# Performance work log

Hardware: AMD Instinct MI355X
Metric: run time of the kernel (lower is better)

## Reference

```python
import jax, jax.numpy as jnp
import numpy as np
import math

N = 50000
E = 600000
HID = 128
NG = 50
NF = 128
CUTOFF = 10.0
OFFSET = 0.0


def ssp(x):
    # shifted softplus, standard SchNet activation
    return jax.nn.softplus(x) - jnp.log(2.0).astype(x.dtype)


def setup_inputs() -> dict:
    key = jax.random.key(0)
    ks = jax.random.split(key, 12)
    x = jax.random.normal(ks[0], (N, HID), dtype=jnp.float32)
    ji_pairs = jax.random.randint(ks[1], (2, E), 0, N, dtype=jnp.int64)
    e_ji = jax.random.uniform(ks[2], (E,), dtype=jnp.float32) * CUTOFF
    e_ji_basis = jax.random.normal(ks[3], (E, NG), dtype=jnp.float32)
    # filter_nn: Linear(NG, NF) -> ssp -> Linear(NF, NF)
    fw1 = jax.random.normal(ks[4], (NF, NG), dtype=jnp.float32) * (1.0 / np.sqrt(NG))
    fb1 = jnp.zeros((NF,), jnp.float32)
    fw2 = jax.random.normal(ks[5], (NF, NF), dtype=jnp.float32) * (1.0 / np.sqrt(NF))
    fb2 = jnp.zeros((NF,), jnp.float32)
    # CFConv linear1 (no bias), linear2
    w1 = jax.random.normal(ks[6], (NF, HID), dtype=jnp.float32) * (1.0 / np.sqrt(HID))
    w2 = jax.random.normal(ks[7], (HID, NF), dtype=jnp.float32) * (1.0 / np.sqrt(NF))
    b2 = jnp.zeros((HID,), jnp.float32)
    # InteractionBlock linear3
    w3 = jax.random.normal(ks[8], (HID, HID), dtype=jnp.float32) * (1.0 / np.sqrt(HID))
    b3 = jnp.zeros((HID,), jnp.float32)
    return {"x": x, "ji_pairs": ji_pairs, "e_ji": e_ji, "e_ji_basis": e_ji_basis,
            "fw1": fw1, "fb1": fb1, "fw2": fw2, "fb2": fb2,
            "w1": w1, "w2": w2, "b2": b2, "w3": w3, "b3": b3}


def reference(x, ji_pairs, e_ji, e_ji_basis, fw1, fb1, fw2, fb2, w1, w2, b2, w3, b3):
    # cosine cutoff  [E]
    C = 0.25 * (jnp.cos((e_ji - OFFSET) * (np.pi / (CUTOFF - OFFSET))) + 1.0)
    # filter MLP on edge basis  [E, NF]
    h = ssp(e_ji_basis @ fw1.T + fb1)
    W = (h @ fw2.T + fb2) * C[:, None]
    # node projection  [N, NF]
    xh = x @ w1.T
    # gather x_j, modulate by W, scatter-add to target nodes (PyG source_to_target)
    src, dst = ji_pairs[0], ji_pairs[1]
    msg = xh[src] * W                                # [E, NF]
    agg = jax.ops.segment_sum(msg, dst, num_segments=N)  # [N, NF]
    out = agg @ w2.T + b2                            # [N, HID]
    out = ssp(out)
    out = out @ w3.T + b3
    return out
```

## Files before the change

kernel.cpp:

```cpp
#include <hip/hip_runtime.h>

typedef float f32x4 __attribute__((ext_vector_type(4)));
typedef short bf16x8 __attribute__((ext_vector_type(8)));
typedef unsigned short u16;
typedef unsigned int u32;

__device__ __forceinline__ u32 cvt_pk_bf16(float lo, float hi) {
    u32 r;
    asm("v_cvt_pk_bf16_f32 %0, %1, %2" : "=v"(r) : "v"(lo), "v"(hi));
    return r;
}

__device__ __forceinline__ u16 f2b(float f) {
    union { float f; u32 u; } v; v.f = f;
    u32 r = v.u + 0x7fffu + ((v.u >> 16) & 1u);
    return (u16)(r >> 16);
}
__device__ __forceinline__ float b2f_lo(u32 p) {
    union { u32 u; float f; } v; v.u = p << 16; return v.f;
}
__device__ __forceinline__ float b2f_hi(u32 p) {
    union { u32 u; float f; } v; v.u = p & 0xffff0000u; return v.f;
}

__device__ __forceinline__ float ssp(float x) {
    return fmaxf(x, 0.0f) + __logf(1.0f + __expf(-fabsf(x))) - 0.6931471805599453f;
}

__global__ void prep_weights(const float* __restrict__ fw1,
                             const float* __restrict__ fw2,
                             const float* __restrict__ w1,
                             const float* __restrict__ w2,
                             const float* __restrict__ w3,
                             u16* __restrict__ out) {
    int t = blockIdx.x * blockDim.x + threadIdx.x;
    if (t < 128 * 64) {
        int c = t >> 6, k = t & 63;
        out[t] = f2b(k < 50 ? fw1[c * 50 + k] : 0.0f);
        return;
    }
    t -= 128 * 64;
    if (t < 16384) { out[8192 + t] = f2b(fw2[t]); return; }
    t -= 16384;
    if (t < 16384) { out[8192 + 16384 + t] = f2b(w1[t]); return; }
    t -= 16384;
    if (t < 16384) { out[8192 + 32768 + t] = f2b(w2[t]); return; }
    t -= 16384;
    if (t < 16384) { out[8192 + 49152 + t] = f2b(w3[t]); return; }
}

template <int ACT, int OBF>
__global__ __launch_bounds__(256, 3) void linear128(
    const float* __restrict__ in, const u16* __restrict__ wb,
    const float* __restrict__ bias, void* __restrict__ outv, int M) {
    __shared__ u16 in_lds[64 * 136];
    __shared__ u16 w_lds[128 * 136];

    const int tid = threadIdx.x;
    const int r0 = blockIdx.x * 64;

    for (int idx = tid; idx < 128 * 16; idx += 256) {
        int c = idx >> 4, kc = (idx & 15) * 8;
        *reinterpret_cast<uint4*>(&w_lds[c * 136 + kc]) =
            *reinterpret_cast<const uint4*>(&wb[c * 128 + kc]);
    }
    for (int idx = tid; idx < 64 * 32; idx += 256) {
        int r = idx >> 5, kc = (idx & 31) * 4;
        int row = r0 + r;
        float4 v = make_float4(0.f, 0.f, 0.f, 0.f);
        if (row < M) v = *reinterpret_cast<const float4*>(&in[(size_t)row * 128 + kc]);
        u32* p = reinterpret_cast<u32*>(&in_lds[r * 136 + kc]);
        p[0] = cvt_pk_bf16(v.x, v.y); p[1] = cvt_pk_bf16(v.z, v.w);
    }
    __syncthreads();

    const int l = tid & 63, w = tid >> 6;
    const int lr = l & 15, lg = l >> 4;

    f32x4 acc[8] = {};
    for (int ks = 0; ks < 4; ++ks) {
        bf16x8 a = *reinterpret_cast<const bf16x8*>(
            &in_lds[(w * 16 + lr) * 136 + ks * 32 + lg * 8]);
        for (int n = 0; n < 8; ++n) {
            bf16x8 b = *reinterpret_cast<const bf16x8*>(
                &w_lds[(n * 16 + lr) * 136 + ks * 32 + lg * 8]);
            acc[n] = __builtin_amdgcn_mfma_f32_16x16x32_bf16(a, b, acc[n], 0, 0, 0);
        }
    }

    for (int n = 0; n < 8; ++n) {
        int c = n * 16 + lr;
        float bv = bias ? bias[c] : 0.0f;
        for (int i = 0; i < 4; ++i) {
            int row = r0 + w * 16 + lg * 4 + i;
            if (row < M) {
                float v = acc[n][i] + bv;
                if (ACT) v = ssp(v);
                if (OBF) ((u16*)outv)[(size_t)row * 128 + c] = f2b(v);
                else     ((float*)outv)[(size_t)row * 128 + c] = v;
            }
        }
    }
}

__global__ __launch_bounds__(512) void edge_mlp(
    const float* __restrict__ basis, const float* __restrict__ e_ji,
    const u16* __restrict__ fw1b, const u16* __restrict__ fw2b,
    const float* __restrict__ fb1, const float* __restrict__ fb2,
    const int* __restrict__ epos, u16* __restrict__ Wb,
    int E, int nTiles, int stride) {
    __shared__ u16 bas[2][32 * 72];
    __shared__ u16 hb[2][32 * 136];

    const int tid = threadIdx.x;
    const int l = tid & 63, w = tid >> 6;
    const int lr = l & 15, lg = l >> 4;
    const int c8 = lg * 8, c4 = lg * 4;

    bf16x8 wa1[2], wa2[4];
    const u16* p1 = &fw1b[(size_t)(w * 16 + lr) * 64];
    wa1[0] = *reinterpret_cast<const bf16x8*>(p1 + c8);
    wa1[1] = *reinterpret_cast<const bf16x8*>(p1 + 32 + c8);
    const u16* p2 = &fw2b[(size_t)(w * 16 + lr) * 128];
#pragma unroll
    for (int ks = 0; ks < 4; ++ks)
        wa2[ks] = *reinterpret_cast<const bf16x8*>(p2 + ks * 32 + c8);
    const float4 b1v = *reinterpret_cast<const float4*>(&fb1[w * 16 + c4]);
    const float4 b2v = *reinterpret_cast<const float4*>(&fb2[w * 16 + c4]);

    for (int idx = tid; idx < 2 * 32 * 7; idx += 512) {
        int b = idx / 224, rem = idx - b * 224;
        int row = rem / 7, q = rem - row * 7;
        *reinterpret_cast<u32*>(&bas[b][row * 72 + 50 + 2 * q]) = 0u;
    }

    const int srow = tid & 31, cb = tid >> 5;
    const bool has2 = cb < 9;

    int it = blockIdx.x;
    if (it >= nTiles) return;

    {
        int er = it * 32 + srow; if (er >= E) er = E - 1;
        const float* rp = &basis[(size_t)er * 50];
        float2 v0 = *reinterpret_cast<const float2*>(rp + 2 * cb);
        *reinterpret_cast<u32*>(&bas[0][srow * 72 + 2 * cb]) = cvt_pk_bf16(v0.x, v0.y);
        if (has2) {
            float2 v1 = *reinterpret_cast<const float2*>(rp + 2 * (cb + 16));
            *reinterpret_cast<u32*>(&bas[0][srow * 72 + 2 * (cb + 16)]) =
                cvt_pk_bf16(v1.x, v1.y);
        }
    }
    __syncthreads();

    int buf = 0;
    for (; it < nTiles; it += stride, buf ^= 1) {
        const int nxt = it + stride;
        const bool hn = nxt < nTiles;
        float2 stg0, stg1;
        if (hn) {
            int er = nxt * 32 + srow; if (er >= E) er = E - 1;
            const float* rp = &basis[(size_t)er * 50];
            stg0 = *reinterpret_cast<const float2*>(rp + 2 * cb);
            if (has2) stg1 = *reinterpret_cast<const float2*>(rp + 2 * (cb + 16));
        }
        const int er0 = it * 32 + lr, er1 = er0 + 16;
        const int ec0 = er0 < E ? er0 : E - 1;
        const int ec1 = er1 < E ? er1 : E - 1;
        const int ep0 = epos[ec0], ep1 = epos[ec1];
        const float ej0 = e_ji[ec0], ej1 = e_ji[ec1];

        f32x4 acc1[2] = {};
#pragma unroll
        for (int ks = 0; ks < 2; ++ks) {
            bf16x8 bb0 = *reinterpret_cast<const bf16x8*>(
                &bas[buf][lr * 72 + ks * 32 + c8]);
            bf16x8 bb1 = *reinterpret_cast<const bf16x8*>(
                &bas[buf][(16 + lr) * 72 + ks * 32 + c8]);
            acc1[0] = __builtin_amdgcn_mfma_f32_16x16x32_bf16(wa1[ks], bb0, acc1[0], 0, 0, 0);
            acc1[1] = __builtin_amdgcn_mfma_f32_16x16x32_bf16(wa1[ks], bb1, acc1[1], 0, 0, 0);
        }
#pragma unroll
        for (int t = 0; t < 2; ++t) {
            u32* d = reinterpret_cast<u32*>(
                &hb[buf][(t * 16 + lr) * 136 + w * 16 + c4]);
            d[0] = cvt_pk_bf16(ssp(acc1[t][0] + b1v.x), ssp(acc1[t][1] + b1v.y));
            d[1] = cvt_pk_bf16(ssp(acc1[t][2] + b1v.z), ssp(acc1[t][3] + b1v.w));
        }
        if (hn) {
            *reinterpret_cast<u32*>(&bas[buf ^ 1][srow * 72 + 2 * cb]) =
                cvt_pk_bf16(stg0.x, stg0.y);
            if (has2)
                *reinterpret_cast<u32*>(&bas[buf ^ 1][srow * 72 + 2 * (cb + 16)]) =
                    cvt_pk_bf16(stg1.x, stg1.y);
        }
        __syncthreads();

        f32x4 acc2[2] = {};
#pragma unroll
        for (int ks = 0; ks < 4; ++ks) {
            bf16x8 hb0 = *reinterpret_cast<const bf16x8*>(
                &hb[buf][lr * 136 + ks * 32 + c8]);
            bf16x8 hb1 = *reinterpret_cast<const bf16x8*>(
                &hb[buf][(16 + lr) * 136 + ks * 32 + c8]);
            acc2[0] = __builtin_amdgcn_mfma_f32_16x16x32_bf16(wa2[ks], hb0, acc2[0], 0, 0, 0);
            acc2[1] = __builtin_amdgcn_mfma_f32_16x16x32_bf16(wa2[ks], hb1, acc2[1], 0, 0, 0);
        }
#pragma unroll
        for (int t = 0; t < 2; ++t) {
            const int er = t == 0 ? er0 : er1;
            if (er < E) {
                const float ej = t == 0 ? ej0 : ej1;
                const int pos = t == 0 ? ep0 : ep1;
                const float cv = 0.25f * (__cosf(ej * 0.31415926535897932f) + 1.0f);
                uint2 pk;
                pk.x = cvt_pk_bf16((acc2[t][0] + b2v.x) * cv,
                                   (acc2[t][1] + b2v.y) * cv);
                pk.y = cvt_pk_bf16((acc2[t][2] + b2v.z) * cv,
                                   (acc2[t][3] + b2v.w) * cv);
                *reinterpret_cast<uint2*>(
                    &Wb[(size_t)pos * 128 + w * 16 + c4]) = pk;
            }
        }
    }
}

__global__ __launch_bounds__(256) void fused_tail(
    const float* __restrict__ agg, const u16* __restrict__ w2b,
    const u16* __restrict__ w3b, const float* __restrict__ b2,
    const float* __restrict__ b3, float* __restrict__ out,
    int N, int nTiles, int stride) {
    __shared__ u16 bas[2][32 * 136];
    __shared__ u16 hb[2][32 * 136];

    const int tid = threadIdx.x;
    const int l = tid & 63, w = tid >> 6;
    const int lr = l & 15, lg = l >> 4;
    const int c8 = lg * 8, c4 = lg * 4;

    bf16x8 wA[2][4], wB[2][4];
    float4 b2v[2], b3v[2];
#pragma unroll
    for (int i = 0; i < 2; ++i) {
        const u16* pA = &w2b[(size_t)((w * 2 + i) * 16 + lr) * 128];
        const u16* pB = &w3b[(size_t)((w * 2 + i) * 16 + lr) * 128];
#pragma unroll
        for (int ks = 0; ks < 4; ++ks) {
            wA[i][ks] = *reinterpret_cast<const bf16x8*>(pA + ks * 32 + c8);
            wB[i][ks] = *reinterpret_cast<const bf16x8*>(pB + ks * 32 + c8);
        }
        b2v[i] = *reinterpret_cast<const float4*>(&b2[(w * 2 + i) * 16 + c4]);
        b3v[i] = *reinterpret_cast<const float4*>(&b3[(w * 2 + i) * 16 + c4]);
    }

    const int srow = tid & 31, cb = tid >> 5;

    int it = blockIdx.x;
    if (it >= nTiles) return;

    {
        int nd = it * 32 + srow; if (nd >= N) nd = N - 1;
        const float* rp = &agg[(size_t)nd * 128];
#pragma unroll
        for (int r = 0; r < 8; ++r) {
            int c = cb + r * 8;
            float2 v = *reinterpret_cast<const float2*>(rp + 2 * c);
            *reinterpret_cast<u32*>(&bas[0][srow * 136 + 2 * c]) =
                cvt_pk_bf16(v.x, v.y);
        }
    }
    __syncthreads();

    int buf = 0;
    for (; it < nTiles; it += stride, buf ^= 1) {
        const int nxt = it + stride;
        const bool hn = nxt < nTiles;
        float2 stg[8];
        if (hn) {
            int nd = nxt * 32 + srow; if (nd >= N) nd = N - 1;
            const float* rp = &agg[(size_t)nd * 128];
#pragma unroll
            for (int r = 0; r < 8; ++r)
                stg[r] = *reinterpret_cast<const float2*>(rp + 2 * (cb + r * 8));
        }

        f32x4 acc1[2][2] = {};
#pragma unroll
        for (int ks = 0; ks < 4; ++ks) {
            bf16x8 bb0 = *reinterpret_cast<const bf16x8*>(
                &bas[buf][lr * 136 + ks * 32 + c8]);
            bf16x8 bb1 = *reinterpret_cast<const bf16x8*>(
                &bas[buf][(16 + lr) * 136 + ks * 32 + c8]);
#pragma unroll
            for (int i = 0; i < 2; ++i) {
                acc1[0][i] = __builtin_amdgcn_mfma_f32_16x16x32_bf16(wA[i][ks], bb0, acc1[0][i], 0, 0, 0);
                acc1[1][i] = __builtin_amdgcn_mfma_f32_16x16x32_bf16(wA[i][ks], bb1, acc1[1][i], 0, 0, 0);
            }
        }
#pragma unroll
        for (int t = 0; t < 2; ++t) {
#pragma unroll
            for (int i = 0; i < 2; ++i) {
                u32* d = reinterpret_cast<u32*>(
                    &hb[buf][(t * 16 + lr) * 136 + (w * 2 + i) * 16 + c4]);
                d[0] = cvt_pk_bf16(ssp(acc1[t][i][0] + b2v[i].x),
                                   ssp(acc1[t][i][1] + b2v[i].y));
                d[1] = cvt_pk_bf16(ssp(acc1[t][i][2] + b2v[i].z),
                                   ssp(acc1[t][i][3] + b2v[i].w));
            }
        }
        if (hn) {
#pragma unroll
            for (int r = 0; r < 8; ++r)
                *reinterpret_cast<u32*>(&bas[buf ^ 1][srow * 136 + 2 * (cb + r * 8)]) =
                    cvt_pk_bf16(stg[r].x, stg[r].y);
        }
        __syncthreads();

        f32x4 acc2[2][2] = {};
#pragma unroll
        for (int ks = 0; ks < 4; ++ks) {
            bf16x8 hb0 = *reinterpret_cast<const bf16x8*>(
                &hb[buf][lr * 136 + ks * 32 + c8]);
            bf16x8 hb1 = *reinterpret_cast<const bf16x8*>(
                &hb[buf][(16 + lr) * 136 + ks * 32 + c8]);
#pragma unroll
            for (int i = 0; i < 2; ++i) {
                acc2[0][i] = __builtin_amdgcn_mfma_f32_16x16x32_bf16(wB[i][ks], hb0, acc2[0][i], 0, 0, 0);
                acc2[1][i] = __builtin_amdgcn_mfma_f32_16x16x32_bf16(wB[i][ks], hb1, acc2[1][i], 0, 0, 0);
            }
        }
#pragma unroll
        for (int t = 0; t < 2; ++t) {
            int nd = it * 32 + t * 16 + lr;
            if (nd < N) {
#pragma unroll
                for (int i = 0; i < 2; ++i) {
                    float4 o;
                    o.x = acc2[t][i][0] + b3v[i].x;
                    o.y = acc2[t][i][1] + b3v[i].y;
                    o.z = acc2[t][i][2] + b3v[i].z;
                    o.w = acc2[t][i][3] + b3v[i].w;
                    *reinterpret_cast<float4*>(
                        &out[(size_t)nd * 128 + (w * 2 + i) * 16 + c4]) = o;
                }
            }
        }
    }
}

__global__ void hist_kernel(const int* __restrict__ pairs, int* __restrict__ deg, int E) {
    int e = blockIdx.x * blockDim.x + threadIdx.x;
    if (e < E) atomicAdd(&deg[pairs[E + e]], 1);
}

__global__ void scan_a(const int* __restrict__ deg, int* __restrict__ incl,
                       int* __restrict__ bsum, int N) {
    __shared__ int s[256];
    int i = blockIdx.x * 256 + threadIdx.x;
    int v = (i < N) ? deg[i] : 0;
    s[threadIdx.x] = v; __syncthreads();
    for (int off = 1; off < 256; off <<= 1) {
        int t = (threadIdx.x >= off) ? s[threadIdx.x - off] : 0;
        __syncthreads();
        s[threadIdx.x] += t; __syncthreads();
    }
    if (i < N) incl[i] = s[threadIdx.x];
    if (threadIdx.x == 255) bsum[blockIdx.x] = s[255];
}

__global__ void scan_b(int* __restrict__ bsum, int nb) {
    __shared__ int s[256];
    int v = (threadIdx.x < nb) ? bsum[threadIdx.x] : 0;
    s[threadIdx.x] = v; __syncthreads();
    for (int off = 1; off < 256; off <<= 1) {
        int t = (threadIdx.x >= off) ? s[threadIdx.x - off] : 0;
        __syncthreads();
        s[threadIdx.x] += t; __syncthreads();
    }
    if (threadIdx.x < nb) bsum[threadIdx.x] = s[threadIdx.x] - v;
}

__global__ void scan_c(const int* __restrict__ incl, const int* __restrict__ deg,
                       const int* __restrict__ bsum, int* __restrict__ rowst,
                       int* __restrict__ cursor, int N) {
    int i = blockIdx.x * 256 + threadIdx.x;
    if (i < N) {
        int r = incl[i] - deg[i] + bsum[blockIdx.x];
        rowst[i] = r; cursor[i] = r;
    }
}

__global__ void fill_kernel(const int* __restrict__ pairs, int* __restrict__ cursor,
                            int* __restrict__ esrc, int* __restrict__ epos, int E) {
    int e = blockIdx.x * blockDim.x + threadIdx.x;
    if (e < E) {
        int s = pairs[e], d = pairs[E + e];
        int pos = atomicAdd(&cursor[d], 1);
        esrc[pos] = s;
        epos[e] = pos;
    }
}

__global__ __launch_bounds__(256) void aggregate(
    const u16* __restrict__ Wb, const u16* __restrict__ xhb,
    const int* __restrict__ rowst, const int* __restrict__ deg,
    const int* __restrict__ esrc, float* __restrict__ agg, int N) {
    const int w = threadIdx.x >> 6, lane = threadIdx.x & 63;
    const int n = blockIdx.x * 4 + w;
    if (n >= N) return;
    const int rs = rowst[n], d = deg[n];
    const int g = lane >> 4;
    const int co = (lane & 15) * 8;
    float acc[8] = {0.f, 0.f, 0.f, 0.f, 0.f, 0.f, 0.f, 0.f};
    const int nq = (d + 3) >> 2;
    const int dm1 = d > 0 ? d - 1 : 0;

    int srcn = (d > 0) ? esrc[rs + (g < d ? g : dm1)] : 0;
    for (int q = 0; q < nq; ++q) {
        const int k = q * 4 + g;
        const bool val = k < d;
        const int row = rs + (val ? k : dm1);
        const int src = srcn;
        const int kn = (q + 1) * 4 + g;
        if (q + 1 < nq) srcn = esrc[rs + (kn < d ? kn : dm1)];

        uint4 wp = *reinterpret_cast<const uint4*>(&Wb[(size_t)row * 128 + co]);
        uint4 xp = *reinterpret_cast<const uint4*>(&xhb[(size_t)src * 128 + co]);
        if (val) {
            const u32* wu = reinterpret_cast<const u32*>(&wp);
            const u32* xu = reinterpret_cast<const u32*>(&xp);
#pragma unroll
            for (int c = 0; c < 4; ++c) {
                acc[2 * c]     = fmaf(b2f_lo(xu[c]), b2f_lo(wu[c]), acc[2 * c]);
                acc[2 * c + 1] = fmaf(b2f_hi(xu[c]), b2f_hi(wu[c]), acc[2 * c + 1]);
            }
        }
    }
#pragma unroll
    for (int c = 0; c < 8; ++c) {
        float v = acc[c];
        v += __shfl_xor(v, 16);
        v += __shfl_xor(v, 32);
        acc[c] = v;
    }
    if (g == 0) {
        float4 o0 = make_float4(acc[0], acc[1], acc[2], acc[3]);
        float4 o1 = make_float4(acc[4], acc[5], acc[6], acc[7]);
        *reinterpret_cast<float4*>(&agg[(size_t)n * 128 + co]) = o0;
        *reinterpret_cast<float4*>(&agg[(size_t)n * 128 + co + 4]) = o1;
    }
}

__global__ __launch_bounds__(256, 2) void edge_kernel(
    const float* __restrict__ basis, const float* __restrict__ e_ji,
    const int* __restrict__ pairs, const float* __restrict__ xh,
    const u16* __restrict__ fw1b, const u16* __restrict__ fw2b,
    const float* __restrict__ fb1, const float* __restrict__ fb2,
    float* __restrict__ agg, int E) {
    __shared__ u16 hb[64 * 136];
    __shared__ u16 fw1_lds[128 * 72];
    __shared__ u16 fw2_lds[128 * 136];
    __shared__ float cc[64];
    __shared__ int s_src[64];
    __shared__ int s_dst[64];

    const int tid = threadIdx.x;
    const int e0 = blockIdx.x * 64;

    for (int idx = tid; idx < 128 * 8; idx += 256) {
        int c = idx >> 3, kc = (idx & 7) * 8;
        *reinterpret_cast<uint4*>(&fw1_lds[c * 72 + kc]) =
            *reinterpret_cast<const uint4*>(&fw1b[c * 64 + kc]);
    }
    for (int idx = tid; idx < 128 * 16; idx += 256) {
        int c = idx >> 4, kc = (idx & 15) * 8;
        *reinterpret_cast<uint4*>(&fw2_lds[c * 136 + kc]) =
            *reinterpret_cast<const uint4*>(&fw2b[c * 128 + kc]);
    }
    for (int idx = tid; idx < 64 * 64; idx += 256) {
        int e = idx >> 6, k = idx & 63;
        int eg = e0 + e;
        float v = (k < 50 && eg < E) ? basis[(size_t)eg * 50 + k] : 0.0f;
        hb[e * 72 + k] = f2b(v);
    }
    if (tid < 64) {
        int eg = e0 + tid;
        if (eg < E) {
            cc[tid] = 0.25f * (__cosf(e_ji[eg] * 0.31415926535897932f) + 1.0f);
            s_src[tid] = pairs[eg];
            s_dst[tid] = pairs[E + eg];
        } else { cc[tid] = 0.0f; s_src[tid] = 0; s_dst[tid] = 0; }
    }
    __syncthreads();

    const int l = tid & 63, w = tid >> 6;
    const int lr = l & 15, lg = l >> 4;

    f32x4 acc1[8] = {};
    for (int ks = 0; ks < 2; ++ks) {
        bf16x8 a = *reinterpret_cast<const bf16x8*>(
            &hb[(w * 16 + lr) * 72 + ks * 32 + lg * 8]);
        for (int n = 0; n < 8; ++n) {
            bf16x8 b = *reinterpret_cast<const bf16x8*>(
                &fw1_lds[(n * 16 + lr) * 72 + ks * 32 + lg * 8]);
            acc1[n] = __builtin_amdgcn_mfma_f32_16x16x32_bf16(a, b, acc1[n], 0, 0, 0);
        }
    }
    __syncthreads();

    for (int n = 0; n < 8; ++n) {
        int c = n * 16 + lr;
        float bv = fb1[c];
        for (int i = 0; i < 4; ++i) {
            int r = w * 16 + lg * 4 + i;
            hb[r * 136 + c] = f2b(ssp(acc1[n][i] + bv));
        }
    }
    __syncthreads();

    f32x4 acc2[8] = {};
    for (int ks = 0; ks < 4; ++ks) {
        bf16x8 a = *reinterpret_cast<const bf16x8*>(
            &hb[(w * 16 + lr) * 136 + ks * 32 + lg * 8]);
        for (int n = 0; n < 8; ++n) {
            bf16x8 b = *reinterpret_cast<const bf16x8*>(
                &fw2_lds[(n * 16 + lr) * 136 + ks * 32 + lg * 8]);
            acc2[n] = __builtin_amdgcn_mfma_f32_16x16x32_bf16(a, b, acc2[n], 0, 0, 0);
        }
    }

    for (int n = 0; n < 8; ++n) {
        int c = n * 16 + lr;
        float bv = fb2[c];
        for (int i = 0; i < 4; ++i) {
            int eloc = w * 16 + lg * 4 + i;
            if (e0 + eloc < E) {
                float Wv = (acc2[n][i] + bv) * cc[eloc];
                float val = xh[(size_t)s_src[eloc] * 128 + c] * Wv;
                unsafeAtomicAdd(&agg[(size_t)s_dst[eloc] * 128 + c], val);
            }
        }
    }
}

extern "C" void kernel_launch(void* const* d_in, const int* in_sizes, int n_in,
                              void* d_out, int out_size, void* d_ws, size_t ws_size,
                              hipStream_t stream) {
    const float* x      = (const float*)d_in[0];
    const int*   pairs  = (const int*)d_in[1];
    const float* e_ji   = (const float*)d_in[2];
    const float* basis  = (const float*)d_in[3];
    const float* fw1    = (const float*)d_in[4];
    const float* fb1    = (const float*)d_in[5];
    const float* fw2    = (const float*)d_in[6];
    const float* fb2    = (const float*)d_in[7];
    const float* w1     = (const float*)d_in[8];
    const float* w2     = (const float*)d_in[9];
    const float* b2     = (const float*)d_in[10];
    const float* w3     = (const float*)d_in[11];
    const float* b3     = (const float*)d_in[12];
    float* out = (float*)d_out;

    const int N = in_sizes[0] / 128;
    const int E = in_sizes[2];
    const int nodeBlocks = (N + 63) / 64;
    const int nchunks = (N + 255) / 256;
    char* ws = (char*)d_ws;

    size_t off = 0;
    auto nxt = [&](size_t bytes) {
        size_t o = off; off = (off + bytes + 255) & ~(size_t)255; return o;
    };
    u16*   Wb     = (u16*)  (ws + nxt((size_t)E * 128 * 2));
    u16*   xhb    = (u16*)  (ws + nxt((size_t)N * 128 * 2));
    float* agg    = (float*)(ws + nxt((size_t)N * 128 * 4));
    u16*   wb     = (u16*)  (ws + nxt(81920 * 2));
    int*   deg    = (int*)  (ws + nxt((size_t)N * 4));
    int*   incl   = (int*)  (ws + nxt((size_t)N * 4));
    int*   rowst  = (int*)  (ws + nxt((size_t)N * 4));
    int*   cursor = (int*)  (ws + nxt((size_t)N * 4));
    int*   bsum   = (int*)  (ws + nxt(1024));
    int*   esrc   = (int*)  (ws + nxt((size_t)E * 4));
    int*   epos   = (int*)  (ws + nxt((size_t)E * 4));
    const size_t needed = off;

    const u16* fw1b = wb;
    const u16* fw2b = wb + 8192;
    const u16* w1b  = wb + 8192 + 16384;
    const u16* w2b  = wb + 8192 + 32768;
    const u16* w3b  = wb + 8192 + 49152;

    if (ws_size >= needed && nchunks <= 256) {
        prep_weights<<<288, 256, 0, stream>>>(fw1, fw2, w1, w2, w3, wb);
        hipMemsetAsync(deg, 0, (size_t)N * 4, stream);

        linear128<0, 1><<<nodeBlocks, 256, 0, stream>>>(x, w1b, nullptr, xhb, N);

        hist_kernel<<<(E + 255) / 256, 256, 0, stream>>>(pairs, deg, E);
        scan_a<<<nchunks, 256, 0, stream>>>(deg, incl, bsum, N);
        scan_b<<<1, 256, 0, stream>>>(bsum, nchunks);
        scan_c<<<nchunks, 256, 0, stream>>>(incl, deg, bsum, rowst, cursor, N);
        fill_kernel<<<(E + 255) / 256, 256, 0, stream>>>(pairs, cursor, esrc, epos, E);

        const int nTiles = (E + 31) / 32;
        const int gridE = nTiles < 1024 ? nTiles : 1024;
        edge_mlp<<<gridE, 512, 0, stream>>>(basis, e_ji, fw1b, fw2b,
                                            fb1, fb2, epos, Wb, E, nTiles, gridE);
        aggregate<<<(N + 3) / 4, 256, 0, stream>>>(Wb, xhb, rowst, deg,
                                                   esrc, agg, N);

        const int ntT = (N + 31) / 32;
        const int gridT = ntT < 1024 ? ntT : 1024;
        fused_tail<<<gridT, 256, 0, stream>>>(agg, w2b, w3b, b2, b3, out,
                                              N, ntT, gridT);
    } else {
        const size_t nodeBytes = (size_t)N * 128 * sizeof(float);
        float* xhf   = (float*)ws;
        float* aggf  = (float*)(ws + nodeBytes);
        u16*   wbf   = (u16*)(ws + 2 * nodeBytes);
        const u16* ffw1b = wbf;
        const u16* ffw2b = wbf + 8192;
        const u16* fw1bw = wbf + 8192 + 16384;
        const u16* fw2bw = wbf + 8192 + 32768;
        const u16* fw3bw = wbf + 8192 + 49152;

        prep_weights<<<288, 256, 0, stream>>>(fw1, fw2, w1, w2, w3, wbf);
        hipMemsetAsync(aggf, 0, nodeBytes, stream);
        linear128<0, 0><<<nodeBlocks, 256, 0, stream>>>(x, fw1bw, nullptr, xhf, N);
        edge_kernel<<<(E + 63) / 64, 256, 0, stream>>>(basis, e_ji, pairs, xhf,
                                                       ffw1b, ffw2b, fb1, fb2, aggf, E);
        linear128<1, 0><<<nodeBlocks, 256, 0, stream>>>(aggf, fw2bw, b2, out, N);
        linear128<0, 0><<<nodeBlocks, 256, 0, stream>>>(out, fw3bw, b3, out, N);
    }
}
```

Before: 276.5 us.

## Fuse CSR aggregation with the two-layer node tail into one kernel

Merges the per-node gather/aggregate kernel with the fused_tail MLP kernel. Each 512-thread block aggregates 32 nodes (4 per wave) into a bf16 LDS tile and then runs the w2/ssp/w3 MFMA chain on it directly. This removes the fp32 agg round trip through global memory and one launch. In exchange it drops the persistent double-buffered tail loop and makes each block finish all of its gather work before any MFMA runs.

```diff
diff --git a/kernel.cpp b/kernel.cpp
--- a/kernel.cpp
+++ b/kernel.cpp
@@ -225,130 +225,6 @@
     }
 }
 
-__global__ __launch_bounds__(256) void fused_tail(
-    const float* __restrict__ agg, const u16* __restrict__ w2b,
-    const u16* __restrict__ w3b, const float* __restrict__ b2,
-    const float* __restrict__ b3, float* __restrict__ out,
-    int N, int nTiles, int stride) {
-    __shared__ u16 bas[2][32 * 136];
-    __shared__ u16 hb[2][32 * 136];
-
-    const int tid = threadIdx.x;
-    const int l = tid & 63, w = tid >> 6;
-    const int lr = l & 15, lg = l >> 4;
-    const int c8 = lg * 8, c4 = lg * 4;
-
-    bf16x8 wA[2][4], wB[2][4];
-    float4 b2v[2], b3v[2];
-#pragma unroll
-    for (int i = 0; i < 2; ++i) {
-        const u16* pA = &w2b[(size_t)((w * 2 + i) * 16 + lr) * 128];
-        const u16* pB = &w3b[(size_t)((w * 2 + i) * 16 + lr) * 128];
-#pragma unroll
-        for (int ks = 0; ks < 4; ++ks) {
-            wA[i][ks] = *reinterpret_cast<const bf16x8*>(pA + ks * 32 + c8);
-            wB[i][ks] = *reinterpret_cast<const bf16x8*>(pB + ks * 32 + c8);
-        }
-        b2v[i] = *reinterpret_cast<const float4*>(&b2[(w * 2 + i) * 16 + c4]);
-        b3v[i] = *reinterpret_cast<const float4*>(&b3[(w * 2 + i) * 16 + c4]);
-    }
-
-    const int srow = tid & 31, cb = tid >> 5;
-
-    int it = blockIdx.x;
-    if (it >= nTiles) return;
-
-    {
-        int nd = it * 32 + srow; if (nd >= N) nd = N - 1;
-        const float* rp = &agg[(size_t)nd * 128];
-#pragma unroll
-        for (int r = 0; r < 8; ++r) {
-            int c = cb + r * 8;
-            float2 v = *reinterpret_cast<const float2*>(rp + 2 * c);
-            *reinterpret_cast<u32*>(&bas[0][srow * 136 + 2 * c]) =
-                cvt_pk_bf16(v.x, v.y);
-        }
-    }
-    __syncthreads();
-
-    int buf = 0;
-    for (; it < nTiles; it += stride, buf ^= 1) {
-        const int nxt = it + stride;
-        const bool hn = nxt < nTiles;
-        float2 stg[8];
-        if (hn) {
-            int nd = nxt * 32 + srow; if (nd >= N) nd = N - 1;
-            const float* rp = &agg[(size_t)nd * 128];
-#pragma unroll
-            for (int r = 0; r < 8; ++r)
-                stg[r] = *reinterpret_cast<const float2*>(rp + 2 * (cb + r * 8));
-        }
-
-        f32x4 acc1[2][2] = {};
-#pragma unroll
-        for (int ks = 0; ks < 4; ++ks) {
-            bf16x8 bb0 = *reinterpret_cast<const bf16x8*>(
-                &bas[buf][lr * 136 + ks * 32 + c8]);
-            bf16x8 bb1 = *reinterpret_cast<const bf16x8*>(
-                &bas[buf][(16 + lr) * 136 + ks * 32 + c8]);
-#pragma unroll
-            for (int i = 0; i < 2; ++i) {
-                acc1[0][i] = __builtin_amdgcn_mfma_f32_16x16x32_bf16(wA[i][ks], bb0, acc1[0][i], 0, 0, 0);
-                acc1[1][i] = __builtin_amdgcn_mfma_f32_16x16x32_bf16(wA[i][ks], bb1, acc1[1][i], 0, 0, 0);
-            }
-        }
-#pragma unroll
-        for (int t = 0; t < 2; ++t) {
-#pragma unroll
-            for (int i = 0; i < 2; ++i) {
-                u32* d = reinterpret_cast<u32*>(
-                    &hb[buf][(t * 16 + lr) * 136 + (w * 2 + i) * 16 + c4]);
-                d[0] = cvt_pk_bf16(ssp(acc1[t][i][0] + b2v[i].x),
-                                   ssp(acc1[t][i][1] + b2v[i].y));
-                d[1] = cvt_pk_bf16(ssp(acc1[t][i][2] + b2v[i].z),
-                                   ssp(acc1[t][i][3] + b2v[i].w));
-            }
-        }
-        if (hn) {
-#pragma unroll
-            for (int r = 0; r < 8; ++r)
-                *reinterpret_cast<u32*>(&bas[buf ^ 1][srow * 136 + 2 * (cb + r * 8)]) =
-                    cvt_pk_bf16(stg[r].x, stg[r].y);
-        }
-        __syncthreads();
-
-        f32x4 acc2[2][2] = {};
-#pragma unroll
-        for (int ks = 0; ks < 4; ++ks) {
-            bf16x8 hb0 = *reinterpret_cast<const bf16x8*>(
-                &hb[buf][lr * 136 + ks * 32 + c8]);
-            bf16x8 hb1 = *reinterpret_cast<const bf16x8*>(
-                &hb[buf][(16 + lr) * 136 + ks * 32 + c8]);
-#pragma unroll
-            for (int i = 0; i < 2; ++i) {
-                acc2[0][i] = __builtin_amdgcn_mfma_f32_16x16x32_bf16(wB[i][ks], hb0, acc2[0][i], 0, 0, 0);
-                acc2[1][i] = __builtin_amdgcn_mfma_f32_16x16x32_bf16(wB[i][ks], hb1, acc2[1][i], 0, 0, 0);
-            }
-        }
-#pragma unroll
-        for (int t = 0; t < 2; ++t) {
-            int nd = it * 32 + t * 16 + lr;
-            if (nd < N) {
-#pragma unroll
-                for (int i = 0; i < 2; ++i) {
-                    float4 o;
-                    o.x = acc2[t][i][0] + b3v[i].x;
-                    o.y = acc2[t][i][1] + b3v[i].y;
-                    o.z = acc2[t][i][2] + b3v[i].z;
-                    o.w = acc2[t][i][3] + b3v[i].w;
-                    *reinterpret_cast<float4*>(
-                        &out[(size_t)nd * 128 + (w * 2 + i) * 16 + c4]) = o;
-                }
-            }
-        }
-    }
-}
-
 __global__ void hist_kernel(const int* __restrict__ pairs, int* __restrict__ deg, int E) {
     int e = blockIdx.x * blockDim.x + threadIdx.x;
     if (e < E) atomicAdd(&deg[pairs[E + e]], 1);
@@ -402,53 +278,129 @@
     }
 }
 
-__global__ __launch_bounds__(256) void aggregate(
+__global__ __launch_bounds__(512) void agg_tail(
     const u16* __restrict__ Wb, const u16* __restrict__ xhb,
     const int* __restrict__ rowst, const int* __restrict__ deg,
-    const int* __restrict__ esrc, float* __restrict__ agg, int N) {
-    const int w = threadIdx.x >> 6, lane = threadIdx.x & 63;
-    const int n = blockIdx.x * 4 + w;
-    if (n >= N) return;
-    const int rs = rowst[n], d = deg[n];
-    const int g = lane >> 4;
-    const int co = (lane & 15) * 8;
-    float acc[8] = {0.f, 0.f, 0.f, 0.f, 0.f, 0.f, 0.f, 0.f};
-    const int nq = (d + 3) >> 2;
-    const int dm1 = d > 0 ? d - 1 : 0;
-
-    int srcn = (d > 0) ? esrc[rs + (g < d ? g : dm1)] : 0;
-    for (int q = 0; q < nq; ++q) {
-        const int k = q * 4 + g;
-        const bool val = k < d;
-        const int row = rs + (val ? k : dm1);
-        const int src = srcn;
-        const int kn = (q + 1) * 4 + g;
-        if (q + 1 < nq) srcn = esrc[rs + (kn < d ? kn : dm1)];
-
-        uint4 wp = *reinterpret_cast<const uint4*>(&Wb[(size_t)row * 128 + co]);
-        uint4 xp = *reinterpret_cast<const uint4*>(&xhb[(size_t)src * 128 + co]);
-        if (val) {
-            const u32* wu = reinterpret_cast<const u32*>(&wp);
-            const u32* xu = reinterpret_cast<const u32*>(&xp);
-#pragma unroll
-            for (int c = 0; c < 4; ++c) {
-                acc[2 * c]     = fmaf(b2f_lo(xu[c]), b2f_lo(wu[c]), acc[2 * c]);
-                acc[2 * c + 1] = fmaf(b2f_hi(xu[c]), b2f_hi(wu[c]), acc[2 * c + 1]);
+    const int* __restrict__ esrc, const u16* __restrict__ w2b,
+    const u16* __restrict__ w3b, const float* __restrict__ b2,
+    const float* __restrict__ b3, float* __restrict__ out, int N) {
+    __shared__ u16 ab[32 * 136];
+    __shared__ u16 hb[32 * 136];
+
+    const int tid = threadIdx.x;
+    const int l = tid & 63, w = tid >> 6;
+    const int lr = l & 15, lg = l >> 4;
+    const int c8 = lg * 8, c4 = lg * 4;
+    const int n0 = blockIdx.x * 32;
+
+    bf16x8 wA[4], wB[4];
+    const u16* pA = &w2b[(size_t)(w * 16 + lr) * 128];
+    const u16* pB = &w3b[(size_t)(w * 16 + lr) * 128];
+#pragma unroll
+    for (int ks = 0; ks < 4; ++ks) {
+        wA[ks] = *reinterpret_cast<const bf16x8*>(pA + ks * 32 + c8);
+        wB[ks] = *reinterpret_cast<const bf16x8*>(pB + ks * 32 + c8);
+    }
+    const float4 b2v = *reinterpret_cast<const float4*>(&b2[w * 16 + c4]);
+    const float4 b3v = *reinterpret_cast<const float4*>(&b3[w * 16 + c4]);
+
+    const int g = lg;
+    const int co = lr * 8;
+
+    int rs4[4], d4[4];
+#pragma unroll
+    for (int i = 0; i < 4; ++i) {
+        int n = n0 + w * 4 + i;
+        int nn = n < N ? n : N - 1;
+        rs4[i] = rowst[nn];
+        d4[i] = deg[nn];
+    }
+
+#pragma unroll
+    for (int i = 0; i < 4; ++i) {
+        const int rs = rs4[i], d = d4[i];
+        const int nq = (d + 3) >> 2;
+        const int dm1 = d > 0 ? d - 1 : 0;
+        float acc[8] = {0.f, 0.f, 0.f, 0.f, 0.f, 0.f, 0.f, 0.f};
+
+        int srcn = (d > 0) ? esrc[rs + (g < d ? g : dm1)] : 0;
+        for (int q = 0; q < nq; ++q) {
+            const int k = q * 4 + g;
+            const bool val = k < d;
+            const int row = rs + (val ? k : dm1);
+            const int src = srcn;
+            const int kn = (q + 1) * 4 + g;
+            if (q + 1 < nq) srcn = esrc[rs + (kn < d ? kn : dm1)];
+
+            uint4 wp = *reinterpret_cast<const uint4*>(&Wb[(size_t)row * 128 + co]);
+            uint4 xp = *reinterpret_cast<const uint4*>(&xhb[(size_t)src * 128 + co]);
+            if (val) {
+                const u32* wu = reinterpret_cast<const u32*>(&wp);
+                const u32* xu = reinterpret_cast<const u32*>(&xp);
+#pragma unroll
+                for (int c = 0; c < 4; ++c) {
+                    acc[2 * c]     = fmaf(b2f_lo(xu[c]), b2f_lo(wu[c]), acc[2 * c]);
+                    acc[2 * c + 1] = fmaf(b2f_hi(xu[c]), b2f_hi(wu[c]), acc[2 * c + 1]);
+                }
             }
         }
-    }
-#pragma unroll
-    for (int c = 0; c < 8; ++c) {
-        float v = acc[c];
-        v += __shfl_xor(v, 16);
-        v += __shfl_xor(v, 32);
-        acc[c] = v;
-    }
-    if (g == 0) {
-        float4 o0 = make_float4(acc[0], acc[1], acc[2], acc[3]);
-        float4 o1 = make_float4(acc[4], acc[5], acc[6], acc[7]);
-        *reinterpret_cast<float4*>(&agg[(size_t)n * 128 + co]) = o0;
-        *reinterpret_cast<float4*>(&agg[(size_t)n * 128 + co + 4]) = o1;
+#pragma unroll
+        for (int c = 0; c < 8; ++c) {
+            float v = acc[c];
+            v += __shfl_xor(v, 16);
+            v += __shfl_xor(v, 32);
+            acc[c] = v;
+        }
+        if (g == 0) {
+            u32* dst = reinterpret_cast<u32*>(&ab[(w * 4 + i) * 136 + co]);
+            dst[0] = cvt_pk_bf16(acc[0], acc[1]);
+            dst[1] = cvt_pk_bf16(acc[2], acc[3]);
+            dst[2] = cvt_pk_bf16(acc[4], acc[5]);
+            dst[3] = cvt_pk_bf16(acc[6], acc[7]);
+        }
+    }
+    __syncthreads();
+
+    f32x4 acc1[2] = {};
+#pragma unroll
+    for (int ks = 0; ks < 4; ++ks) {
+        bf16x8 bb0 = *reinterpret_cast<const bf16x8*>(
+            &ab[lr * 136 + ks * 32 + c8]);
+        bf16x8 bb1 = *reinterpret_cast<const bf16x8*>(
+            &ab[(16 + lr) * 136 + ks * 32 + c8]);
+        acc1[0] = __builtin_amdgcn_mfma_f32_16x16x32_bf16(wA[ks], bb0, acc1[0], 0, 0, 0);
+        acc1[1] = __builtin_amdgcn_mfma_f32_16x16x32_bf16(wA[ks], bb1, acc1[1], 0, 0, 0);
+    }
+#pragma unroll
+    for (int t = 0; t < 2; ++t) {
+        u32* d = reinterpret_cast<u32*>(
+            &hb[(t * 16 + lr) * 136 + w * 16 + c4]);
+        d[0] = cvt_pk_bf16(ssp(acc1[t][0] + b2v.x), ssp(acc1[t][1] + b2v.y));
+        d[1] = cvt_pk_bf16(ssp(acc1[t][2] + b2v.z), ssp(acc1[t][3] + b2v.w));
+    }
+    __syncthreads();
+
+    f32x4 acc2[2] = {};
+#pragma unroll
+    for (int ks = 0; ks < 4; ++ks) {
+        bf16x8 hb0 = *reinterpret_cast<const bf16x8*>(
+            &hb[lr * 136 + ks * 32 + c8]);
+        bf16x8 hb1 = *reinterpret_cast<const bf16x8*>(
+            &hb[(16 + lr) * 136 + ks * 32 + c8]);
+        acc2[0] = __builtin_amdgcn_mfma_f32_16x16x32_bf16(wB[ks], hb0, acc2[0], 0, 0, 0);
+        acc2[1] = __builtin_amdgcn_mfma_f32_16x16x32_bf16(wB[ks], hb1, acc2[1], 0, 0, 0);
+    }
+#pragma unroll
+    for (int t = 0; t < 2; ++t) {
+        const int nd = n0 + t * 16 + lr;
+        if (nd < N) {
+            float4 o;
+            o.x = acc2[t][0] + b3v.x;
+            o.y = acc2[t][1] + b3v.y;
+            o.z = acc2[t][2] + b3v.z;
+            o.w = acc2[t][3] + b3v.w;
+            *reinterpret_cast<float4*>(&out[(size_t)nd * 128 + w * 16 + c4]) = o;
+        }
     }
 }
 
@@ -607,13 +559,10 @@
         const int gridE = nTiles < 1024 ? nTiles : 1024;
         edge_mlp<<<gridE, 512, 0, stream>>>(basis, e_ji, fw1b, fw2b,
                                             fb1, fb2, epos, Wb, E, nTiles, gridE);
-        aggregate<<<(N + 3) / 4, 256, 0, stream>>>(Wb, xhb, rowst, deg,
-                                                   esrc, agg, N);
 
         const int ntT = (N + 31) / 32;
-        const int gridT = ntT < 1024 ? ntT : 1024;
-        fused_tail<<<gridT, 256, 0, stream>>>(agg, w2b, w3b, b2, b3, out,
-                                              N, ntT, gridT);
+        agg_tail<<<ntT, 512, 0, stream>>>(Wb, xhb, rowst, deg, esrc,
+                                          w2b, w3b, b2, b3, out, N);
     } else {
         const size_t nodeBytes = (size_t)N * 128 * sizeof(float);
         float* xhf   = (float*)ws;
```

Measured after the change: 281.8 us. Within noise of the previous version (+1.9%).
